# Kernel tuning notes

Hardware: AMD Instinct MI355X
Metric: run time of the kernel (lower is better)

Reference implementation:

```python
import jax, jax.numpy as jnp
import numpy as np

EPS_LN = 1e-6
EPS_POOL = 1e-6
GAMMA = 2.0

def _layernorm(x, w, b):
    mu = jnp.mean(x, axis=-1, keepdims=True)
    var = jnp.mean((x - mu) ** 2, axis=-1, keepdims=True)
    return (x - mu) * jax.lax.rsqrt(var + EPS_LN) * w + b

def setup_inputs() -> dict:
    key = jax.random.key(0)
    k1, k2, k3 = jax.random.split(key, 3)
    B, N, d = 16, 8192, 768
    x = jax.random.normal(k1, (B, N, d), dtype=jnp.float32)
    ln_w = jnp.ones((d,), dtype=jnp.float32)
    ln_b = jnp.zeros((d,), dtype=jnp.float32)
    wq = jax.random.normal(k2, (d, d), dtype=jnp.float32) * (d ** -0.5)
    wk = jax.random.normal(k3, (d, d), dtype=jnp.float32) * (d ** -0.5)
    return {"x": x, "ln_w": ln_w, "ln_b": ln_b, "wq": wq, "wk": wk}

def reference(x, ln_w, ln_b, wq, wk):
    B, N, d = x.shape
    num_heads = 1
    head_dim = d // num_heads
    scale = head_dim ** -0.5
    # GAP query [B,1,d]
    q = jnp.mean(x, axis=1, keepdims=True)
    # normalized patches serve as both k and v
    kv = _layernorm(x, ln_w, ln_b)           # [B,N,d]
    qq = q @ wq.T                             # [B,1,d]
    kk = kv @ wk.T                            # [B,N,d]
    # single-query attention (num_heads=1 so head reshape is identity)
    logits = jnp.einsum("bqd,bnd->bqn", qq, kk) * scale  # [B,1,N]
    attn = jax.nn.softmax(logits, axis=-1)
    # GeM power-mean pooling: global min shift keeps base positive
    vp = (kv - jnp.min(kv) + EPS_POOL) ** GAMMA           # [B,N,d]
    out = jnp.einsum("bqn,bnd->bqd", attn, vp) ** (1.0 / GAMMA)  # [B,1,d]
    return jnp.squeeze(out, axis=1)           # [B,d]
```

## Files before the change

### kernel.cpp

```cpp
#include <hip/hip_runtime.h>
#include <math.h>

#define B_SZ    16
#define N_ROWS  8192
#define D       768
#define EPS_LN  1e-6f
#define EPS_POOL 1e-6f
#define SCALE   0.03608439182435161f

#define ROWS_PER_BLOCK 64
#define ROWS_PER_WAVE  16
#define BLOCKS_PER_B   (N_ROWS / ROWS_PER_BLOCK)
#define NBLK_PASS      (B_SZ * BLOCKS_PER_B)

#define WS_COLSUM   0
#define WS_R        (WS_COLSUM + B_SZ*D)
#define WS_QQ       (WS_R + B_SZ*D)
#define WS_GMIN     (WS_QQ + B_SZ*D)
#define WS_PART     (WS_GMIN + 32)
#define PART_STRIDE 1544

__device__ __forceinline__ void atomicMinFloat(unsigned int* addr, float val) {
    if (val >= 0.0f) atomicMin((int*)addr, __float_as_int(val));
    else             atomicMax(addr, __float_as_uint(val));
}

__global__ __launch_bounds__(256) void k0_init(float* __restrict__ ws) {
    int i = blockIdx.x * 256 + threadIdx.x;
    if (i < 2 * B_SZ * D) ws[i] = 0.0f;
    if (i == 0) ((unsigned int*)ws)[WS_GMIN] = 0x7F800000u;
}

__global__ __launch_bounds__(256) void ka_colsum(const float* __restrict__ x,
                                                 float* __restrict__ ws) {
    __shared__ float lds[4][D];
    const int tid  = threadIdx.x;
    const int lane = tid & 63;
    const int wv   = tid >> 6;
    const int b    = blockIdx.x >> 7;
    const int chunk= blockIdx.x & 127;
    const int n0   = chunk * ROWS_PER_BLOCK + wv * ROWS_PER_WAVE;
    const float* base = x + ((size_t)b * N_ROWS + n0) * D + 4*lane;

    float cs[12];
    #pragma unroll
    for (int k = 0; k < 12; ++k) cs[k] = 0.0f;

    for (int i = 0; i < ROWS_PER_WAVE; ++i) {
        const float* row = base + (size_t)i * D;
        #pragma unroll
        for (int g = 0; g < 3; ++g) {
            const float4 v = *(const float4*)(row + 256*g);
            cs[4*g]   += v.x; cs[4*g+1] += v.y;
            cs[4*g+2] += v.z; cs[4*g+3] += v.w;
        }
    }
    #pragma unroll
    for (int g = 0; g < 3; ++g)
        *(float4*)&lds[wv][4*lane + 256*g] =
            make_float4(cs[4*g], cs[4*g+1], cs[4*g+2], cs[4*g+3]);
    __syncthreads();

    float* colsum = ws + WS_COLSUM + (size_t)b * D;
    #pragma unroll
    for (int k = 0; k < 3; ++k) {
        const int c = tid + 256*k;
        atomicAdd(&colsum[c], lds[0][c] + lds[1][c] + lds[2][c] + lds[3][c]);
    }
}

__global__ __launch_bounds__(256) void kb1_qq(const float* __restrict__ wq,
                                              float* __restrict__ ws) {
    __shared__ float q[D];
    const int tid  = threadIdx.x;
    const int lane = tid & 63;
    const int wv   = tid >> 6;
    const int b    = blockIdx.x / 12;
    const int ic   = blockIdx.x % 12;

    const float* colsum = ws + WS_COLSUM + (size_t)b * D;
    for (int c = tid; c < D; c += 256) q[c] = colsum[c] * (1.0f / N_ROWS);
    __syncthreads();

    for (int k = 0; k < 16; ++k) {
        const int i = ic * 64 + wv * 16 + k;
        const float* row = wq + (size_t)i * D + 4*lane;
        float p = 0.0f;
        #pragma unroll
        for (int g = 0; g < 3; ++g) {
            const float4 a = *(const float4*)(row + 256*g);
            const int c = 4*lane + 256*g;
            p += a.x*q[c] + a.y*q[c+1] + a.z*q[c+2] + a.w*q[c+3];
        }
        #pragma unroll
        for (int off = 32; off; off >>= 1) p += __shfl_xor(p, off);
        if (lane == 0) ws[WS_QQ + (size_t)b * D + i] = p * SCALE;
    }
}

__global__ __launch_bounds__(256) void kb2_r(const float* __restrict__ wk,
                                             float* __restrict__ ws) {
    __shared__ float qs[16][48];
    const int tid = threadIdx.x;
    const int jt  = blockIdx.x / 16;
    const int ic  = blockIdx.x % 16;

    #pragma unroll
    for (int k = 0; k < 3; ++k) {
        const int v  = tid + 256*k;
        const int bb = v / 48, ii = v % 48;
        qs[bb][ii] = ws[WS_QQ + (size_t)bb * D + ic*48 + ii];
    }
    __syncthreads();

    float acc[16];
    #pragma unroll
    for (int bb = 0; bb < 16; ++bb) acc[bb] = 0.0f;

    const int j = jt * 256 + tid;
    for (int i = 0; i < 48; ++i) {
        const float wkv = wk[(size_t)(ic*48 + i) * D + j];
        #pragma unroll
        for (int bb = 0; bb < 16; ++bb) acc[bb] += qs[bb][i] * wkv;
    }
    #pragma unroll
    for (int bb = 0; bb < 16; ++bb)
        atomicAdd(&ws[WS_R + (size_t)bb * D + j], acc[bb]);
}

__global__ __launch_bounds__(256) void kc_fused(const float* __restrict__ x,
                                                const float* __restrict__ lnw,
                                                const float* __restrict__ lnb,
                                                float* __restrict__ ws) {
    __shared__ float lds_acc[4][2*D];
    __shared__ float lds_ms[4], lds_se[4], lds_min[4];
    const int tid  = threadIdx.x;
    const int lane = tid & 63;
    const int wv   = tid >> 6;
    const int b    = blockIdx.x >> 7;
    const int chunk= blockIdx.x & 127;
    const int n0   = chunk * ROWS_PER_BLOCK + wv * ROWS_PER_WAVE;

    float w[12], cb[12], rw[12];
    float A = 0.0f, C = 0.0f;
    {
        const float* rb = ws + WS_R + (size_t)b * D + 4*lane;
        #pragma unroll
        for (int g = 0; g < 3; ++g) {
            const float4 vw = *(const float4*)(lnw + 4*lane + 256*g);
            const float4 vc = *(const float4*)(lnb + 4*lane + 256*g);
            const float4 vr = *(const float4*)(rb + 256*g);
            w[4*g]=vw.x; w[4*g+1]=vw.y; w[4*g+2]=vw.z; w[4*g+3]=vw.w;
            cb[4*g]=vc.x; cb[4*g+1]=vc.y; cb[4*g+2]=vc.z; cb[4*g+3]=vc.w;
            rw[4*g]  =vr.x*vw.x; rw[4*g+1]=vr.y*vw.y;
            rw[4*g+2]=vr.z*vw.z; rw[4*g+3]=vr.w*vw.w;
            C += vr.x*vc.x + vr.y*vc.y + vr.z*vc.z + vr.w*vc.w;
        }
        #pragma unroll
        for (int k = 0; k < 12; ++k) A += rw[k];
        #pragma unroll
        for (int off = 32; off; off >>= 1) {
            A += __shfl_xor(A, off); C += __shfl_xor(C, off);
        }
    }

    float m = -INFINITY, se = 0.0f, kvmin = INFINITY;
    float a1[12], a2[12];
    #pragma unroll
    for (int k = 0; k < 12; ++k) { a1[k] = 0.0f; a2[k] = 0.0f; }

    const float* base = x + ((size_t)b * N_ROWS + n0) * D + 4*lane;

    for (int i = 0; i < ROWS_PER_WAVE; ++i) {
        float xv[12];
        {
            const float* row = base + (size_t)i * D;
            #pragma unroll
            for (int g = 0; g < 3; ++g) {
                const float4 v = *(const float4*)(row + 256*g);
                xv[4*g]=v.x; xv[4*g+1]=v.y; xv[4*g+2]=v.z; xv[4*g+3]=v.w;
            }
        }
        float s = 0.0f, ss = 0.0f, dt = 0.0f;
        #pragma unroll
        for (int k = 0; k < 12; ++k) {
            s += xv[k]; ss += xv[k]*xv[k]; dt += rw[k]*xv[k];
        }
        #pragma unroll
        for (int off = 32; off; off >>= 1) {
            s  += __shfl_xor(s,  off);
            ss += __shfl_xor(ss, off);
            dt += __shfl_xor(dt, off);
        }
        const float mu   = s * (1.0f / D);
        const float var  = ss * (1.0f / D) - mu * mu;
        const float rstd = rsqrtf(var + EPS_LN);
        const float logit = rstd * (dt - mu * A) + C;

        if (logit > m) {
            const float f = __expf(m - logit);
            se *= f;
            #pragma unroll
            for (int k = 0; k < 12; ++k) { a1[k] *= f; a2[k] *= f; }
            m = logit;
        }
        const float p = __expf(logit - m);
        se += p;

        #pragma unroll
        for (int k = 0; k < 12; ++k) {
            const float kv = (xv[k] - mu) * rstd * w[k] + cb[k];
            kvmin = fminf(kvmin, kv);
            const float u = p * kv;
            a1[k] += u;
            a2[k] += u * kv;
        }
    }

    if (lane == 0) lds_ms[wv] = m;
    __syncthreads();
    const float M = fmaxf(fmaxf(lds_ms[0], lds_ms[1]), fmaxf(lds_ms[2], lds_ms[3]));
    const float f = __expf(m - M);

    #pragma unroll
    for (int g = 0; g < 3; ++g) {
        *(float4*)&lds_acc[wv][4*lane + 256*g] =
            make_float4(a1[4*g]*f, a1[4*g+1]*f, a1[4*g+2]*f, a1[4*g+3]*f);
        *(float4*)&lds_acc[wv][D + 4*lane + 256*g] =
            make_float4(a2[4*g]*f, a2[4*g+1]*f, a2[4*g+2]*f, a2[4*g+3]*f);
    }
    #pragma unroll
    for (int off = 32; off; off >>= 1) kvmin = fminf(kvmin, __shfl_xor(kvmin, off));
    if (lane == 0) { lds_se[wv] = se * f; lds_min[wv] = kvmin; }
    __syncthreads();

    float* part = ws + WS_PART + (size_t)blockIdx.x * PART_STRIDE;
    if (tid == 0) {
        part[0] = M;
        part[1] = lds_se[0] + lds_se[1] + lds_se[2] + lds_se[3];
        atomicMinFloat((unsigned int*)ws + WS_GMIN,
                       fminf(fminf(lds_min[0], lds_min[1]), fminf(lds_min[2], lds_min[3])));
    }
    #pragma unroll
    for (int k = 0; k < 6; ++k) {
        const int idx = tid + 256*k;
        part[8 + idx] = lds_acc[0][idx] + lds_acc[1][idx] + lds_acc[2][idx] + lds_acc[3][idx];
    }
}

__global__ __launch_bounds__(128) void kd_combine(const float* __restrict__ ws,
                                                  float* __restrict__ out) {
    __shared__ float lds_f[128];
    __shared__ float red[4];
    const int tid  = threadIdx.x;
    const int lane = tid & 63;
    const int wv   = tid >> 6;
    const int b    = blockIdx.x / 6;
    const int jt   = blockIdx.x % 6;
    const float* pb = ws + WS_PART + (size_t)b * BLOCKS_PER_B * PART_STRIDE;

    const float mc = pb[(size_t)tid * PART_STRIDE + 0];
    const float sc = pb[(size_t)tid * PART_STRIDE + 1];

    float M = mc;
    #pragma unroll
    for (int off = 32; off; off >>= 1) M = fmaxf(M, __shfl_xor(M, off));
    if (lane == 0) red[wv] = M;
    __syncthreads();
    M = fmaxf(red[0], red[1]);

    const float fc = __expf(mc - M);
    float fs = fc * sc;
    #pragma unroll
    for (int off = 32; off; off >>= 1) fs += __shfl_xor(fs, off);
    if (lane == 0) red[2 + wv] = fs;
    lds_f[tid] = fc;
    __syncthreads();
    const float S = red[2] + red[3];
    const float G = __uint_as_float(((const unsigned int*)ws)[WS_GMIN]) - EPS_POOL;

    const int d = jt * 128 + tid;
    float A1 = 0.0f, A2 = 0.0f;
    for (int c = 0; c < BLOCKS_PER_B; ++c) {
        const float* p = pb + (size_t)c * PART_STRIDE;
        const float w = lds_f[c];
        A1 += w * p[8 + d];
        A2 += w * p[8 + D + d];
    }
    const float e1 = A1 / S;
    const float e2 = A2 / S;
    const float v  = e2 - 2.0f * G * e1 + G * G;
    out[(size_t)b * D + d] = sqrtf(fmaxf(v, 0.0f));
}

extern "C" void kernel_launch(void* const* d_in, const int* in_sizes, int n_in,
                              void* d_out, int out_size, void* d_ws, size_t ws_size,
                              hipStream_t stream) {
    const float* x   = (const float*)d_in[0];
    const float* lnw = (const float*)d_in[1];
    const float* lnb = (const float*)d_in[2];
    const float* wq  = (const float*)d_in[3];
    const float* wk  = (const float*)d_in[4];
    float* ws  = (float*)d_ws;
    float* out = (float*)d_out;

    hipLaunchKernelGGL(k0_init,   dim3(96),        dim3(256), 0, stream, ws);
    hipLaunchKernelGGL(ka_colsum, dim3(NBLK_PASS), dim3(256), 0, stream, x, ws);
    hipLaunchKernelGGL(kb1_qq,    dim3(192),       dim3(256), 0, stream, wq, ws);
    hipLaunchKernelGGL(kb2_r,     dim3(48),        dim3(256), 0, stream, wk, ws);
    hipLaunchKernelGGL(kc_fused,  dim3(NBLK_PASS), dim3(256), 0, stream, x, lnw, lnb, ws);
    hipLaunchKernelGGL(kd_combine,dim3(96),        dim3(128), 0, stream, ws, out);
}
```

Before: 646.4 us.

## Move LayerNorm stats and min to first pass, factor affine out of accumulation

```diff
diff --git a/kernel.cpp b/kernel.cpp
--- a/kernel.cpp
+++ b/kernel.cpp
@@ -17,13 +17,16 @@
 #define WS_R        (WS_COLSUM + B_SZ*D)
 #define WS_QQ       (WS_R + B_SZ*D)
 #define WS_GMIN     (WS_QQ + B_SZ*D)
-#define WS_PART     (WS_GMIN + 32)
+#define WS_STAT     (WS_GMIN + 32)
+#define WS_PART     (WS_STAT + 2*B_SZ*N_ROWS)
 #define PART_STRIDE 1544
 
 __device__ __forceinline__ void atomicMinFloat(unsigned int* addr, float val) {
     if (val >= 0.0f) atomicMin((int*)addr, __float_as_int(val));
     else             atomicMax(addr, __float_as_uint(val));
 }
+__device__ __forceinline__ float hsum4(float4 v)  { return (v.x + v.y) + (v.z + v.w); }
+__device__ __forceinline__ float hsumsq4(float4 v){ return (v.x*v.x + v.y*v.y) + (v.z*v.z + v.w*v.w); }
 
 __global__ __launch_bounds__(256) void k0_init(float* __restrict__ ws) {
     int i = blockIdx.x * 256 + threadIdx.x;
@@ -31,9 +34,12 @@
     if (i == 0) ((unsigned int*)ws)[WS_GMIN] = 0x7F800000u;
 }
 
-__global__ __launch_bounds__(256) void ka_colsum(const float* __restrict__ x,
-                                                 float* __restrict__ ws) {
+__global__ __launch_bounds__(256) void ka_stats(const float* __restrict__ x,
+                                                const float* __restrict__ lnw,
+                                                const float* __restrict__ lnb,
+                                                float* __restrict__ ws) {
     __shared__ float lds[4][D];
+    __shared__ float wvmin[4];
     const int tid  = threadIdx.x;
     const int lane = tid & 63;
     const int wv   = tid >> 6;
@@ -42,19 +48,58 @@
     const int n0   = chunk * ROWS_PER_BLOCK + wv * ROWS_PER_WAVE;
     const float* base = x + ((size_t)b * N_ROWS + n0) * D + 4*lane;
 
+    float w[12], cb[12];
+    #pragma unroll
+    for (int g = 0; g < 3; ++g) {
+        const float4 vw = *(const float4*)(lnw + 4*lane + 256*g);
+        const float4 vc = *(const float4*)(lnb + 4*lane + 256*g);
+        w[4*g]=vw.x; w[4*g+1]=vw.y; w[4*g+2]=vw.z; w[4*g+3]=vw.w;
+        cb[4*g]=vc.x; cb[4*g+1]=vc.y; cb[4*g+2]=vc.z; cb[4*g+3]=vc.w;
+    }
+
     float cs[12];
     #pragma unroll
     for (int k = 0; k < 12; ++k) cs[k] = 0.0f;
+    float kvmin = INFINITY;
+
+    float2* stat = (float2*)(ws + WS_STAT) + (size_t)b * N_ROWS;
 
     for (int i = 0; i < ROWS_PER_WAVE; ++i) {
+        const int n = n0 + i;
         const float* row = base + (size_t)i * D;
+        float xv[12];
+        float s = 0.0f, ss = 0.0f;
         #pragma unroll
         for (int g = 0; g < 3; ++g) {
             const float4 v = *(const float4*)(row + 256*g);
-            cs[4*g]   += v.x; cs[4*g+1] += v.y;
-            cs[4*g+2] += v.z; cs[4*g+3] += v.w;
-        }
-    }
+            xv[4*g]=v.x; xv[4*g+1]=v.y; xv[4*g+2]=v.z; xv[4*g+3]=v.w;
+            s  += hsum4(v);
+            ss += hsumsq4(v);
+        }
+        #pragma unroll
+        for (int off = 32; off; off >>= 1) {
+            s  += __shfl_xor(s,  off);
+            ss += __shfl_xor(ss, off);
+        }
+        const float mu   = s * (1.0f / D);
+        const float var  = ss * (1.0f / D) - mu * mu;
+        const float rstd = rsqrtf(var + EPS_LN);
+        const float rmu  = rstd * mu;
+        if (lane == 0) stat[n] = make_float2(rstd, rmu);
+
+        #pragma unroll
+        for (int k = 0; k < 12; ++k) {
+            cs[k] += xv[k];
+            const float z  = rstd * xv[k] - rmu;
+            const float kv = z * w[k] + cb[k];
+            kvmin = fminf(kvmin, kv);
+        }
+    }
+
+    #pragma unroll
+    for (int off = 32; off; off >>= 1) kvmin = fminf(kvmin, __shfl_xor(kvmin, off));
+    if (lane == 0) wvmin[wv] = kvmin;
+
     #pragma unroll
     for (int g = 0; g < 3; ++g)
         *(float4*)&lds[wv][4*lane + 256*g] =
@@ -66,6 +111,10 @@
     for (int k = 0; k < 3; ++k) {
         const int c = tid + 256*k;
         atomicAdd(&colsum[c], lds[0][c] + lds[1][c] + lds[2][c] + lds[3][c]);
+    }
+    if (tid == 0) {
+        float m = fminf(fminf(wvmin[0], wvmin[1]), fminf(wvmin[2], wvmin[3]));
+        atomicMinFloat((unsigned int*)ws + WS_GMIN, m);
     }
 }
 
@@ -133,23 +182,24 @@
                                                 const float* __restrict__ lnb,
                                                 float* __restrict__ ws) {
     __shared__ float lds_acc[4][2*D];
-    __shared__ float lds_ms[4], lds_se[4], lds_min[4];
+    __shared__ float lds_ms[4], lds_se[4];
     const int tid  = threadIdx.x;
     const int lane = tid & 63;
     const int wv   = tid >> 6;
-    const int b    = blockIdx.x >> 7;
-    const int chunk= blockIdx.x & 127;
+    const int rb   = (NBLK_PASS - 1) - blockIdx.x;
+    const int b    = rb >> 7;
+    const int chunk= rb & 127;
     const int n0   = chunk * ROWS_PER_BLOCK + wv * ROWS_PER_WAVE;
 
     float w[12], cb[12], rw[12];
     float A = 0.0f, C = 0.0f;
     {
-        const float* rb = ws + WS_R + (size_t)b * D + 4*lane;
+        const float* rbase = ws + WS_R + (size_t)b * D + 4*lane;
         #pragma unroll
         for (int g = 0; g < 3; ++g) {
             const float4 vw = *(const float4*)(lnw + 4*lane + 256*g);
             const float4 vc = *(const float4*)(lnb + 4*lane + 256*g);
-            const float4 vr = *(const float4*)(rb + 256*g);
+            const float4 vr = *(const float4*)(rbase + 256*g);
             w[4*g]=vw.x; w[4*g+1]=vw.y; w[4*g+2]=vw.z; w[4*g+3]=vw.w;
             cb[4*g]=vc.x; cb[4*g+1]=vc.y; cb[4*g+2]=vc.z; cb[4*g+3]=vc.w;
             rw[4*g]  =vr.x*vw.x; rw[4*g+1]=vr.y*vw.y;
@@ -164,44 +214,38 @@
         }
     }
 
-    float m = -INFINITY, se = 0.0f, kvmin = INFINITY;
-    float a1[12], a2[12];
-    #pragma unroll
-    for (int k = 0; k < 12; ++k) { a1[k] = 0.0f; a2[k] = 0.0f; }
+    float m = -INFINITY, se = 0.0f;
+    float T1[12], T2[12];
+    #pragma unroll
+    for (int k = 0; k < 12; ++k) { T1[k] = 0.0f; T2[k] = 0.0f; }
 
     const float* base = x + ((size_t)b * N_ROWS + n0) * D + 4*lane;
+    const float2* stat = (const float2*)(ws + WS_STAT) + (size_t)b * N_ROWS;
 
     for (int i = 0; i < ROWS_PER_WAVE; ++i) {
+        const int n = n0 + i;
+        const float2 st = stat[n];
         float xv[12];
+        float dt = 0.0f;
         {
             const float* row = base + (size_t)i * D;
             #pragma unroll
             for (int g = 0; g < 3; ++g) {
                 const float4 v = *(const float4*)(row + 256*g);
                 xv[4*g]=v.x; xv[4*g+1]=v.y; xv[4*g+2]=v.z; xv[4*g+3]=v.w;
+                dt += rw[4*g]*v.x + rw[4*g+1]*v.y + rw[4*g+2]*v.z + rw[4*g+3]*v.w;
             }
         }
-        float s = 0.0f, ss = 0.0f, dt = 0.0f;
-        #pragma unroll
-        for (int k = 0; k < 12; ++k) {
-            s += xv[k]; ss += xv[k]*xv[k]; dt += rw[k]*xv[k];
-        }
-        #pragma unroll
-        for (int off = 32; off; off >>= 1) {
-            s  += __shfl_xor(s,  off);
-            ss += __shfl_xor(ss, off);
-            dt += __shfl_xor(dt, off);
-        }
-        const float mu   = s * (1.0f / D);
-        const float var  = ss * (1.0f / D) - mu * mu;
-        const float rstd = rsqrtf(var + EPS_LN);
-        const float logit = rstd * (dt - mu * A) + C;
+        #pragma unroll
+        for (int off = 32; off; off >>= 1) dt += __shfl_xor(dt, off);
+
+        const float logit = fmaf(st.x, dt, fmaf(-st.y, A, C));
 
         if (logit > m) {
             const float f = __expf(m - logit);
             se *= f;
             #pragma unroll
-            for (int k = 0; k < 12; ++k) { a1[k] *= f; a2[k] *= f; }
+            for (int k = 0; k < 12; ++k) { T1[k] *= f; T2[k] *= f; }
             m = logit;
         }
         const float p = __expf(logit - m);
@@ -209,11 +253,10 @@
 
         #pragma unroll
         for (int k = 0; k < 12; ++k) {
-            const float kv = (xv[k] - mu) * rstd * w[k] + cb[k];
-            kvmin = fminf(kvmin, kv);
-            const float u = p * kv;
-            a1[k] += u;
-            a2[k] += u * kv;
+            const float z = fmaf(st.x, xv[k], -st.y);
+            const float u = p * z;
+            T1[k] += u;
+            T2[k] = fmaf(u, z, T2[k]);
         }
     }
 
@@ -223,23 +266,21 @@
     const float f = __expf(m - M);
 
     #pragma unroll
-    for (int g = 0; g < 3; ++g) {
-        *(float4*)&lds_acc[wv][4*lane + 256*g] =
-            make_float4(a1[4*g]*f, a1[4*g+1]*f, a1[4*g+2]*f, a1[4*g+3]*f);
-        *(float4*)&lds_acc[wv][D + 4*lane + 256*g] =
-            make_float4(a2[4*g]*f, a2[4*g+1]*f, a2[4*g+2]*f, a2[4*g+3]*f);
-    }
-    #pragma unroll
-    for (int off = 32; off; off >>= 1) kvmin = fminf(kvmin, __shfl_xor(kvmin, off));
-    if (lane == 0) { lds_se[wv] = se * f; lds_min[wv] = kvmin; }
-    __syncthreads();
-
-    float* part = ws + WS_PART + (size_t)blockIdx.x * PART_STRIDE;
+    for (int k = 0; k < 12; ++k) {
+        const float cbS = cb[k] * se;
+        const float a1  = fmaf(w[k], T1[k], cbS);
+        const float a2  = fmaf(w[k]*w[k], T2[k],
+                          fmaf(2.0f*w[k]*cb[k], T1[k], cb[k]*cbS));
+        lds_acc[wv][(k/4)*256 + 4*lane + (k&3)]     = a1 * f;
+        lds_acc[wv][D + (k/4)*256 + 4*lane + (k&3)] = a2 * f;
+    }
+    if (lane == 0) lds_se[wv] = se * f;
+    __syncthreads();
+
+    float* part = ws + WS_PART + (size_t)rb * PART_STRIDE;
     if (tid == 0) {
         part[0] = M;
         part[1] = lds_se[0] + lds_se[1] + lds_se[2] + lds_se[3];
-        atomicMinFloat((unsigned int*)ws + WS_GMIN,
-                       fminf(fminf(lds_min[0], lds_min[1]), fminf(lds_min[2], lds_min[3])));
     }
     #pragma unroll
     for (int k = 0; k < 6; ++k) {
@@ -305,7 +346,7 @@
     float* out = (float*)d_out;
 
     hipLaunchKernelGGL(k0_init,   dim3(96),        dim3(256), 0, stream, ws);
-    hipLaunchKernelGGL(ka_colsum, dim3(NBLK_PASS), dim3(256), 0, stream, x, ws);
+    hipLaunchKernelGGL(ka_stats,  dim3(NBLK_PASS), dim3(256), 0, stream, x, lnw, lnb, ws);
     hipLaunchKernelGGL(kb1_qq,    dim3(192),       dim3(256), 0, stream, wq, ws);
     hipLaunchKernelGGL(kb2_r,     dim3(48),        dim3(256), 0, stream, wk, ws);
     hipLaunchKernelGGL(kc_fused,  dim3(NBLK_PASS), dim3(256), 0, stream, x, lnw, lnb, ws);
```

Measured after the change: 651.7 us. Within noise of the previous version (+0.8%).
